# Kernel optimization log

Measured on AMD Instinct MI355X. Metric: run time of the kernel, lower is better.

The kernel has to match this reference:

```python
import jax, jax.numpy as jnp
import numpy as np
import math

H = 8
E = 512
D_K = E // H
NEG = -1000000000.0
# last (and only surviving) row of dist_bar: one threshold per head
DIST_BAR = np.array([0.2, 0.3, 0.4, 0.5, 0.6, 0.7, 0.8, 0.9], dtype=np.float32)


def setup_inputs() -> dict:
    key = jax.random.key(0)
    ks = jax.random.split(key, 12)
    B, N = 8, 1024
    s = 1.0 / math.sqrt(E)
    inp = {
        "query": jax.random.normal(ks[0], (B, N, E), jnp.float32),
        "key": jax.random.normal(ks[1], (B, N, E), jnp.float32),
        "value": jax.random.normal(ks[2], (B, N, E), jnp.float32),
        "dist": jax.random.uniform(ks[3], (B, 1, N, N), jnp.float32),
        "mask": jnp.ones((B, N, N), jnp.int32),
        "Wq": jax.random.normal(ks[4], (E, E), jnp.float32) * s,
        "bq": jnp.zeros((E,), jnp.float32),
        "Wk": jax.random.normal(ks[5], (E, E), jnp.float32) * s,
        "bk": jnp.zeros((E,), jnp.float32),
        "Wv": jax.random.normal(ks[6], (E, E), jnp.float32) * s,
        "bv": jnp.zeros((E,), jnp.float32),
        "Wo": jax.random.normal(ks[7], (E, E), jnp.float32) * s,
        "bo": jnp.zeros((E,), jnp.float32),
    }
    return inp


def reference(query, key, value, dist, mask, Wq, bq, Wk, bk, Wv, bv, Wo, bo):
    B, N, _ = query.shape
    # project and split heads: [B, H, N, D_K]
    def heads(x, W, b):
        return (x @ W.T + b).reshape(B, N, H, D_K).transpose(0, 2, 1, 3)
    q = heads(query, Wq, bq)
    k = heads(key, Wk, bk)
    v = heads(value, Wv, bv)
    scores = jnp.einsum("bhqd,bhkd->bhqk", q, k) / math.sqrt(D_K)
    # padding mask: [B,N,N] -> [B,1,N,N]
    scores = jnp.where(mask[:, None, :, :] == 0, NEG, scores)
    # per-head distance mask: dist [B,1,N,N] < thr[h] -> [B,H,N,N]
    thr = jnp.asarray(DIST_BAR)[None, :, None, None]
    dmask = dist < thr
    # first row/col (global atom) always attend
    dmask = dmask.at[:, :, 0, :].set(True).at[:, :, :, 0].set(True)
    scores = jnp.where(dmask, scores, NEG)
    p = jax.nn.softmax(scores, axis=-1)
    out = jnp.einsum("bhqk,bhkd->bhqd", p, v)  # [B,H,N,D_K]
    out = out.transpose(0, 2, 1, 3).reshape(B, N, H * D_K)
    return out @ Wo.T + bo
```

## Files before the change

### kernel.cpp

```cpp
#include <hip/hip_runtime.h>
#include <stdint.h>


typedef __attribute__((ext_vector_type(8))) short short8;
typedef __attribute__((ext_vector_type(4))) float floatx4;

#define MFMA16(a, b, c) __builtin_amdgcn_mfma_f32_16x16x32_bf16((a), (b), (c), 0, 0, 0)

static __device__ __forceinline__ unsigned short f2bf(float f) {
  union { float f; unsigned u; } v; v.f = f;
  unsigned r = v.u + 0x7fffu + ((v.u >> 16) & 1u);
  return (unsigned short)(r >> 16);
}

static __device__ __forceinline__ void gload_lds16(const void* g, void* l) {
  __builtin_amdgcn_global_load_lds((const __attribute__((address_space(1))) unsigned int*)g,
                                   (__attribute__((address_space(3))) unsigned int*)l,
                                   16, 0, 0);
}
static __device__ __forceinline__ int xsw(int row) { return (row & 3) ^ ((row >> 2) & 3); }

__global__ void codes_kernel(const float* __restrict__ dist, const int* __restrict__ mask,
                             unsigned char* __restrict__ codesP,
                             const float* __restrict__ Wq, const float* __restrict__ Wk,
                             const float* __restrict__ Wv, const float* __restrict__ Wo,
                             unsigned short* __restrict__ o0, unsigned short* __restrict__ o1,
                             unsigned short* __restrict__ o2, unsigned short* __restrict__ o3) {
  if (blockIdx.x >= 8192) {
    int i = (blockIdx.x - 8192) * blockDim.x + threadIdx.x;
    int w = i >> 16, loc = i & 65535;
    const float* s = (w == 0) ? Wq : (w == 1) ? Wk : (w == 2) ? Wv : Wo;
    unsigned short* d = (w == 0) ? o0 : (w == 1) ? o1 : (w == 2) ? o2 : o3;
    float4 v = ((const float4*)s)[loc];
    ushort4 o;
    o.x = f2bf(v.x); o.y = f2bf(v.y); o.z = f2bf(v.z); o.w = f2bf(v.w);
    ((ushort4*)d)[loc] = o;
    return;
  }
  int t = blockIdx.x * blockDim.x + threadIdx.x;
  int flat = t << 2;
  int b = flat >> 20;
  int rem = flat & ((1 << 20) - 1);
  int row = rem >> 10;
  int col0 = rem & 1023;
  float4 d4 = ((const float4*)dist)[t];
  int4 m4 = ((const int4*)mask)[t];
  float dv[4] = {d4.x, d4.y, d4.z, d4.w};
  int mv[4] = {m4.x, m4.y, m4.z, m4.w};
  int rg = row >> 5;
  int st = (row >> 4) & 1;
  int c = row & 15;
  size_t rowbase = (size_t)(b * 32 + rg) * 32768;
  int kt = col0 >> 7;
  int colk = col0 & 127;
  int ci = colk >> 4;
  int hi = (colk >> 2) & 3;
  int lane = hi * 16 + c;
  unsigned pack = 0;
#pragma unroll
  for (int u = 0; u < 4; u++) {
    int col = col0 + u;
    float d = dv[u];
    int hmin = (d >= 0.2f) + (d >= 0.3f) + (d >= 0.4f) + (d >= 0.5f) +
               (d >= 0.6f) + (d >= 0.7f) + (d >= 0.8f) + (d >= 0.9f);
    unsigned cc = (unsigned)hmin;
    if (row == 0 || col == 0) cc = 0;
    if (mv[u] == 0) cc = 9;
    pack |= cc << (u * 8);
  }
  *(unsigned*)&codesP[rowbase + (size_t)kt * 4096 + lane * 64 + st * 32 + ci * 4] = pack;
}

__global__ __launch_bounds__(256) void qkv_gemm(
    const float* __restrict__ Aq, const float* __restrict__ Ak, const float* __restrict__ Av,
    const unsigned short* __restrict__ Wqp, const unsigned short* __restrict__ Wkp,
    const unsigned short* __restrict__ Wvp,
    const float* __restrict__ bq, const float* __restrict__ bk, const float* __restrict__ bv,
    unsigned short* __restrict__ Qh, unsigned short* __restrict__ Kh,
    unsigned short* __restrict__ Vt) {
  const int z = blockIdx.z;
  const float* A = (z == 0) ? Aq : (z == 1) ? Ak : Av;
  const unsigned short* W = (z == 0) ? Wqp : (z == 1) ? Wkp : Wvp;
  const float* bias = (z == 0) ? bq : (z == 1) ? bk : bv;
  unsigned short* O = (z == 0) ? Qh : (z == 1) ? Kh : Vt;

  __shared__ __align__(16) short As[64 * 40];
  __shared__ __align__(16) short Bs[128 * 32];
  const int tid = threadIdx.x;
  const int lane = tid & 63;
  const int wave = tid >> 6;
  const int c = lane & 15;
  const int q = lane >> 4;
  const int m0 = blockIdx.x * 64;
  const int n0 = blockIdx.y * 128;
  const int wr = (wave >> 1) * 32;
  const int wc = (wave & 1) * 64;

  floatx4 acc[2][4];
#pragma unroll
  for (int i = 0; i < 2; i++)
#pragma unroll
    for (int j = 0; j < 4; j++) acc[i][j] = (floatx4)(0.0f);

  const int arow = tid >> 2, ach = tid & 3;
  const float* Ab = A + (size_t)(m0 + arow) * 512 + ach * 8;

  for (int k0 = 0; k0 < 512; k0 += 32) {
    __syncthreads();
#pragma unroll
    for (int it = 0; it < 2; it++) {
      int slot = wave * 128 + it * 64 + lane;
      int brow = slot >> 2, bch = slot & 3;
      int g = bch ^ xsw(brow);
      gload_lds16(W + (size_t)(n0 + brow) * 512 + k0 + g * 8,
                  &Bs[(size_t)(wave * 128 + it * 64) * 8]);
    }
    float4 a0 = *(const float4*)(Ab + k0);
    float4 a1 = *(const float4*)(Ab + k0 + 4);
    short8 av;
    av[0] = (short)f2bf(a0.x); av[1] = (short)f2bf(a0.y);
    av[2] = (short)f2bf(a0.z); av[3] = (short)f2bf(a0.w);
    av[4] = (short)f2bf(a1.x); av[5] = (short)f2bf(a1.y);
    av[6] = (short)f2bf(a1.z); av[7] = (short)f2bf(a1.w);
    *(short8*)(&As[arow * 40 + ach * 8]) = av;
    __syncthreads();

    short8 af[2], bfv[4];
#pragma unroll
    for (int i = 0; i < 2; i++)
      af[i] = *(const short8*)(&As[(wr + i * 16 + c) * 40 + q * 8]);
#pragma unroll
    for (int j = 0; j < 4; j++) {
      int row = wc + j * 16 + c;
      bfv[j] = *(const short8*)(&Bs[row * 32 + (q ^ xsw(row)) * 8]);
    }
#pragma unroll
    for (int i = 0; i < 2; i++)
#pragma unroll
      for (int j = 0; j < 4; j++)
        acc[i][j] = MFMA16(af[i], bfv[j], acc[i][j]);
  }

#pragma unroll
  for (int i = 0; i < 2; i++) {
    int gm0 = m0 + wr + i * 16 + q * 4;
#pragma unroll
    for (int j = 0; j < 4; j++) {
      int gn = n0 + wc + j * 16 + c;
      float bb = bias[gn];
      int h = gn >> 6, d = gn & 63;
      if (z == 2) {
        int b = gm0 >> 10, n = gm0 & 1023;
        ushort4 pk;
#pragma unroll
        for (int r = 0; r < 4; r++) pk[r] = f2bf(acc[i][j][r] + bb);
        *(ushort4*)(&Vt[(((size_t)(b * 8 + h) * 64 + d) << 10) + n]) = pk;
      } else {
#pragma unroll
        for (int r = 0; r < 4; r++) {
          int m = gm0 + r;
          int b = m >> 10, n = m & 1023;
          O[((((size_t)(b * 8 + h)) << 10) + n) * 64 + d] = f2bf(acc[i][j][r] + bb);
        }
      }
    }
  }
}

__global__ __launch_bounds__(256) void out_gemm(const unsigned short* __restrict__ A,
                                                const unsigned short* __restrict__ W,
                                                const float* __restrict__ bias,
                                                float* __restrict__ Out) {
  __shared__ __align__(16) short As[64 * 32];
  __shared__ __align__(16) short Bs[128 * 32];
  const int tid = threadIdx.x;
  const int lane = tid & 63;
  const int wave = tid >> 6;
  const int c = lane & 15;
  const int q = lane >> 4;
  const int m0 = blockIdx.x * 64;
  const int n0 = blockIdx.y * 128;
  const int wr = (wave >> 1) * 32;
  const int wc = (wave & 1) * 64;

  floatx4 acc[2][4];
#pragma unroll
  for (int i = 0; i < 2; i++)
#pragma unroll
    for (int j = 0; j < 4; j++) acc[i][j] = (floatx4)(0.0f);

  for (int k0 = 0; k0 < 512; k0 += 32) {
    __syncthreads();
    {
      int slot = wave * 64 + lane;
      int arow = slot >> 2, ach = slot & 3;
      int g = ach ^ xsw(arow);
      gload_lds16(A + (size_t)(m0 + arow) * 512 + k0 + g * 8, &As[(size_t)(wave * 64) * 8]);
    }
#pragma unroll
    for (int it = 0; it < 2; it++) {
      int slot = wave * 128 + it * 64 + lane;
      int brow = slot >> 2, bch = slot & 3;
      int g = bch ^ xsw(brow);
      gload_lds16(W + (size_t)(n0 + brow) * 512 + k0 + g * 8,
                  &Bs[(size_t)(wave * 128 + it * 64) * 8]);
    }
    __syncthreads();

    short8 af[2], bfv[4];
#pragma unroll
    for (int i = 0; i < 2; i++) {
      int row = wr + i * 16 + c;
      af[i] = *(const short8*)(&As[row * 32 + (q ^ xsw(row)) * 8]);
    }
#pragma unroll
    for (int j = 0; j < 4; j++) {
      int row = wc + j * 16 + c;
      bfv[j] = *(const short8*)(&Bs[row * 32 + (q ^ xsw(row)) * 8]);
    }
#pragma unroll
    for (int i = 0; i < 2; i++)
#pragma unroll
      for (int j = 0; j < 4; j++)
        acc[i][j] = MFMA16(af[i], bfv[j], acc[i][j]);
  }

#pragma unroll
  for (int i = 0; i < 2; i++) {
    int gm0 = m0 + wr + i * 16 + q * 4;
#pragma unroll
    for (int j = 0; j < 4; j++) {
      int gn = n0 + wc + j * 16 + c;
      float bb = bias[gn];
#pragma unroll
      for (int r = 0; r < 4; r++)
        Out[(size_t)(gm0 + r) * 512 + gn] = acc[i][j][r] + bb;
    }
  }
}

__global__ __launch_bounds__(256, 3) void attn_kernel(const unsigned short* __restrict__ Qh,
                                                      const unsigned short* __restrict__ Kh,
                                                      const unsigned short* __restrict__ Vt,
                                                      const unsigned char* __restrict__ codesP,
                                                      unsigned short* __restrict__ AO) {
  __shared__ __align__(16) unsigned short P[4][32 * 132];
  const int tid = threadIdx.x;
  const int lane = tid & 63;
  const int wave = tid >> 6;
  const int wsub = wave & 1;
  const int whalf = wave >> 1;
  const int c = lane & 15;
  const int q = lane >> 4;
  const int bid = blockIdx.x;
  const int swz = ((bid & 7) << 7) | (bid >> 3);
  const int bh = swz >> 4;
  const int gx = swz & 15;
  const int b = bh >> 3;
  const int h = bh & 7;
  const size_t base = (size_t)bh << 16;
  const int rbase = gx * 64 + wsub * 32;
  const int rg = rbase >> 5;
  unsigned short* Pw = &P[wave][0];

  short8 aq[2][2];
#pragma unroll
  for (int st = 0; st < 2; st++)
#pragma unroll
    for (int kk = 0; kk < 2; kk++)
      aq[st][kk] = *(const short8*)(Qh + base + (size_t)(rbase + st * 16 + c) * 64 + kk * 32 + q * 8);

  const unsigned char* cbt = codesP + (size_t)(b * 32 + rg) * 32768 + lane * 64;
  const unsigned short* Kb = Kh + base;
  const unsigned short* Vb = Vt + base;

  float rsum[2] = {0.0f, 0.0f};
  floatx4 o[2][4];
#pragma unroll
  for (int st = 0; st < 2; st++)
#pragma unroll
    for (int ci = 0; ci < 4; ci++) o[st][ci] = (floatx4)(0.0f);

  short8 bk00, bk01, bk10, bk11;
  {
    const unsigned short* Kt0 = Kb + (size_t)(whalf * 4) * 8192;
    bk00 = *(const short8*)(Kt0 + (size_t)(0 * 16 + c) * 64 + 0 * 32 + q * 8);
    bk01 = *(const short8*)(Kt0 + (size_t)(0 * 16 + c) * 64 + 1 * 32 + q * 8);
    bk10 = *(const short8*)(Kt0 + (size_t)(1 * 16 + c) * 64 + 0 * 32 + q * 8);
    bk11 = *(const short8*)(Kt0 + (size_t)(1 * 16 + c) * 64 + 1 * 32 + q * 8);
  }

#pragma unroll
  for (int ph = 0; ph < 16; ph++) {
    const int kt = whalf * 4 + (ph >> 2);
    const int j = ph & 3;
    const unsigned char* cp = cbt + (size_t)kt * 4096;

    short8 vv0 = *(const short8*)(Vb + (size_t)(0 * 16 + c) * 1024 + kt * 128 + j * 32 + q * 8);
    short8 vv1 = *(const short8*)(Vb + (size_t)(1 * 16 + c) * 1024 + kt * 128 + j * 32 + q * 8);
    short8 vv2 = *(const short8*)(Vb + (size_t)(2 * 16 + c) * 1024 + kt * 128 + j * 32 + q * 8);
    short8 vv3 = *(const short8*)(Vb + (size_t)(3 * 16 + c) * 1024 + kt * 128 + j * 32 + q * 8);
    uint2 cw0 = *(const uint2*)(cp + j * 8);
    uint2 cw1 = *(const uint2*)(cp + 32 + j * 8);

    floatx4 s2[2][2];
    s2[0][0] = (floatx4)(0.0f); s2[0][1] = (floatx4)(0.0f);
    s2[1][0] = (floatx4)(0.0f); s2[1][1] = (floatx4)(0.0f);
    s2[0][0] = MFMA16(bk00, aq[0][0], s2[0][0]);
    s2[1][0] = MFMA16(bk00, aq[1][0], s2[1][0]);
    s2[0][0] = MFMA16(bk01, aq[0][1], s2[0][0]);
    s2[1][0] = MFMA16(bk01, aq[1][1], s2[1][0]);
    s2[0][1] = MFMA16(bk10, aq[0][0], s2[0][1]);
    s2[1][1] = MFMA16(bk10, aq[1][0], s2[1][1]);
    s2[0][1] = MFMA16(bk11, aq[0][1], s2[0][1]);
    s2[1][1] = MFMA16(bk11, aq[1][1], s2[1][1]);

    if (ph < 15) {
      const int phn = ph + 1;
      const int ktn = whalf * 4 + (phn >> 2);
      const int jn = phn & 3;
      const unsigned short* Ktn = Kb + (size_t)ktn * 8192;
      bk00 = *(const short8*)(Ktn + (size_t)((2 * jn + 0) * 16 + c) * 64 + 0 * 32 + q * 8);
      bk01 = *(const short8*)(Ktn + (size_t)((2 * jn + 0) * 16 + c) * 64 + 1 * 32 + q * 8);
      bk10 = *(const short8*)(Ktn + (size_t)((2 * jn + 1) * 16 + c) * 64 + 0 * 32 + q * 8);
      bk11 = *(const short8*)(Ktn + (size_t)((2 * jn + 1) * 16 + c) * 64 + 1 * 32 + q * 8);
    }

#pragma unroll
    for (int st = 0; st < 2; st++) {
#pragma unroll
      for (int u = 0; u < 2; u++) {
        unsigned w = st ? (u ? cw1.y : cw1.x) : (u ? cw0.y : cw0.x);
        float ev[4];
#pragma unroll
        for (int r = 0; r < 4; r++) {
          int code = (w >> (r * 8)) & 0xff;
          float ee = (h >= code) ? exp2f(s2[st][u][r] * 0.1803368801111362f) : 0.0f;
          rsum[st] += ee;
          ev[r] = ee;
        }
        unsigned p0, p1;
        asm("v_cvt_pk_bf16_f32 %0, %1, %2" : "=v"(p0) : "v"(ev[0]), "v"(ev[1]));
        asm("v_cvt_pk_bf16_f32 %0, %1, %2" : "=v"(p1) : "v"(ev[2]), "v"(ev[3]));
        uint2 pk; pk.x = p0; pk.y = p1;
        *(uint2*)(&Pw[(st * 16 + c) * 132 + (2 * j + u) * 16 + q * 4]) = pk;
      }
    }

    __builtin_amdgcn_sched_barrier(0);

    short8 ap0 = *(const short8*)(&Pw[(size_t)c * 132 + j * 32 + q * 8]);
    short8 ap1 = *(const short8*)(&Pw[(size_t)(16 + c) * 132 + j * 32 + q * 8]);
    o[0][0] = MFMA16(ap0, vv0, o[0][0]);
    o[1][0] = MFMA16(ap1, vv0, o[1][0]);
    o[0][1] = MFMA16(ap0, vv1, o[0][1]);
    o[1][1] = MFMA16(ap1, vv1, o[1][1]);
    o[0][2] = MFMA16(ap0, vv2, o[0][2]);
    o[1][2] = MFMA16(ap1, vv2, o[1][2]);
    o[0][3] = MFMA16(ap0, vv3, o[0][3]);
    o[1][3] = MFMA16(ap1, vv3, o[1][3]);
  }

  float* Pf = (float*)&P[0][0];
  __syncthreads();
  if (whalf == 1) {
#pragma unroll
    for (int st = 0; st < 2; st++)
#pragma unroll
      for (int ci = 0; ci < 4; ci++)
        *(floatx4*)&Pf[(((wsub * 9 + st * 4 + ci) * 64) + lane) * 4] = o[st][ci];
    float2 rr; rr.x = rsum[0]; rr.y = rsum[1];
    *(float2*)&Pf[(((wsub * 9 + 8) * 64) + lane) * 4] = rr;
  }
  __syncthreads();
  if (whalf == 1) return;

#pragma unroll
  for (int st = 0; st < 2; st++)
#pragma unroll
    for (int ci = 0; ci < 4; ci++) {
      floatx4 p = *(const floatx4*)&Pf[(((wsub * 9 + st * 4 + ci) * 64) + lane) * 4];
      o[st][ci] += p;
    }
  {
    float2 pr = *(const float2*)&Pf[(((wsub * 9 + 8) * 64) + lane) * 4];
    rsum[0] += pr.x; rsum[1] += pr.y;
  }

  float inv2[2];
#pragma unroll
  for (int st = 0; st < 2; st++) {
    float v = rsum[st];
    v += __shfl_xor(v, 16);
    v += __shfl_xor(v, 32);
    inv2[st] = 1.0f / v;
  }
  const int sb = (lane & 48) + ((lane & 48) >> 2);
  float iv[2][4];
#pragma unroll
  for (int st = 0; st < 2; st++)
#pragma unroll
    for (int r = 0; r < 4; r++) iv[st][r] = __shfl(inv2[st], sb + r);

#pragma unroll
  for (int st = 0; st < 2; st++)
#pragma unroll
    for (int r = 0; r < 4; r++) {
      int n = rbase + st * 16 + q * 4 + r;
      size_t ob = ((size_t)((b << 10) + n)) * 512 + h * 64;
#pragma unroll
      for (int ci = 0; ci < 4; ci++)
        AO[ob + ci * 16 + c] = f2bf(o[st][ci][r] * iv[st][r]);
    }
}

extern "C" void kernel_launch(void* const* d_in, const int* in_sizes, int n_in,
                              void* d_out, int out_size, void* d_ws, size_t ws_size,
                              hipStream_t stream) {
  const float* query = (const float*)d_in[0];
  const float* key_  = (const float*)d_in[1];
  const float* value = (const float*)d_in[2];
  const float* dist  = (const float*)d_in[3];
  const int*   mask  = (const int*)d_in[4];
  const float* Wq = (const float*)d_in[5];
  const float* bq = (const float*)d_in[6];
  const float* Wk = (const float*)d_in[7];
  const float* bk = (const float*)d_in[8];
  const float* Wv = (const float*)d_in[9];
  const float* bv = (const float*)d_in[10];
  const float* Wo = (const float*)d_in[11];
  const float* bo = (const float*)d_in[12];

  char* ws = (char*)d_ws;
  size_t off = 0;
  auto alloc = [&](size_t bytes) -> char* {
    char* p = ws + off;
    off += (bytes + 255) & ~(size_t)255;
    return p;
  };
  const size_t NQKV = 8192ull * 512;
  unsigned short* wq16 = (unsigned short*)alloc(512ull * 512 * 2);
  unsigned short* wk16 = (unsigned short*)alloc(512ull * 512 * 2);
  unsigned short* wv16 = (unsigned short*)alloc(512ull * 512 * 2);
  unsigned short* wo16 = (unsigned short*)alloc(512ull * 512 * 2);
  unsigned short* Qh = (unsigned short*)alloc(NQKV * 2);
  unsigned short* Kh = (unsigned short*)alloc(NQKV * 2);
  unsigned short* Vt = (unsigned short*)alloc(NQKV * 2);
  unsigned short* AO = (unsigned short*)alloc(NQKV * 2);
  unsigned char*  codesP = (unsigned char*)alloc(8ull * 1024 * 1024);

  codes_kernel<<<9216, 256, 0, stream>>>(dist, mask, codesP, Wq, Wk, Wv, Wo,
                                         wq16, wk16, wv16, wo16);
  qkv_gemm<<<dim3(128, 4, 3), 256, 0, stream>>>(query, key_, value, wq16, wk16, wv16,
                                                bq, bk, bv, Qh, Kh, Vt);
  attn_kernel<<<1024, 256, 0, stream>>>(Qh, Kh, Vt, codesP, AO);
  out_gemm<<<dim3(128, 4), 256, 0, stream>>>(AO, wo16, bo, (float*)d_out);
}
```

Baseline: 277.4 us.

## Pre-convert QKV inputs to bf16 and coalesce codes writes through LDS

The prep kernel now also converts the query, key and value activations to bf16 in a separate pass. This lets qkv_gemm load its A tiles straight into LDS with global_load_lds and a swizzled layout, instead of converting fp32 in registers each k-step, so A is converted once rather than once per N-block. The codes computation is restructured so each block builds a 4 KB tile in shared memory and writes it out contiguously instead of scattering 4-byte stores. The cost is an extra bf16 copy of the inputs written to and read back from memory, plus extra workspace.

After: 275.7 us, median of 2. No clear change (-0.6%).

```diff
diff --git a/kernel.cpp b/kernel.cpp
--- a/kernel.cpp
+++ b/kernel.cpp
@@ -20,14 +20,36 @@
 }
 static __device__ __forceinline__ int xsw(int row) { return (row & 3) ^ ((row >> 2) & 3); }
 
-__global__ void codes_kernel(const float* __restrict__ dist, const int* __restrict__ mask,
-                             unsigned char* __restrict__ codesP,
-                             const float* __restrict__ Wq, const float* __restrict__ Wk,
-                             const float* __restrict__ Wv, const float* __restrict__ Wo,
-                             unsigned short* __restrict__ o0, unsigned short* __restrict__ o1,
-                             unsigned short* __restrict__ o2, unsigned short* __restrict__ o3) {
-  if (blockIdx.x >= 8192) {
-    int i = (blockIdx.x - 8192) * blockDim.x + threadIdx.x;
+__global__ void prep_kernel(const float* __restrict__ dist, const int* __restrict__ mask,
+                            unsigned char* __restrict__ codesP,
+                            const float* __restrict__ Wq, const float* __restrict__ Wk,
+                            const float* __restrict__ Wv, const float* __restrict__ Wo,
+                            unsigned short* __restrict__ o0, unsigned short* __restrict__ o1,
+                            unsigned short* __restrict__ o2, unsigned short* __restrict__ o3,
+                            const float* __restrict__ Qf, const float* __restrict__ Kf,
+                            const float* __restrict__ Vf,
+                            unsigned short* __restrict__ Qb, unsigned short* __restrict__ Kb,
+                            unsigned short* __restrict__ Vb) {
+  const int tid = threadIdx.x;
+  const unsigned bx = blockIdx.x;
+  if (bx >= 3072) {
+    int j = bx - 3072;
+    int arr = j >> 11;
+    const float* s = (arr == 0) ? Qf : (arr == 1) ? Kf : Vf;
+    unsigned short* d = (arr == 0) ? Qb : (arr == 1) ? Kb : Vb;
+    int idx = (j & 2047) * 256 + tid;
+    float4 v0 = ((const float4*)s)[idx * 2];
+    float4 v1 = ((const float4*)s)[idx * 2 + 1];
+    short8 o;
+    o[0] = (short)f2bf(v0.x); o[1] = (short)f2bf(v0.y);
+    o[2] = (short)f2bf(v0.z); o[3] = (short)f2bf(v0.w);
+    o[4] = (short)f2bf(v1.x); o[5] = (short)f2bf(v1.y);
+    o[6] = (short)f2bf(v1.z); o[7] = (short)f2bf(v1.w);
+    *(short8*)(d + (size_t)idx * 8) = o;
+    return;
+  }
+  if (bx >= 2048) {
+    int i = (bx - 2048) * 256 + tid;
     int w = i >> 16, loc = i & 65535;
     const float* s = (w == 0) ? Wq : (w == 1) ? Wk : (w == 2) ? Wv : Wo;
     unsigned short* d = (w == 0) ? o0 : (w == 1) ? o1 : (w == 2) ? o2 : o3;
@@ -37,54 +59,61 @@
     ((ushort4*)d)[loc] = o;
     return;
   }
-  int t = blockIdx.x * blockDim.x + threadIdx.x;
-  int flat = t << 2;
-  int b = flat >> 20;
-  int rem = flat & ((1 << 20) - 1);
-  int row = rem >> 10;
-  int col0 = rem & 1023;
-  float4 d4 = ((const float4*)dist)[t];
-  int4 m4 = ((const int4*)mask)[t];
-  float dv[4] = {d4.x, d4.y, d4.z, d4.w};
-  int mv[4] = {m4.x, m4.y, m4.z, m4.w};
-  int rg = row >> 5;
-  int st = (row >> 4) & 1;
-  int c = row & 15;
-  size_t rowbase = (size_t)(b * 32 + rg) * 32768;
-  int kt = col0 >> 7;
-  int colk = col0 & 127;
-  int ci = colk >> 4;
-  int hi = (colk >> 2) & 3;
-  int lane = hi * 16 + c;
-  unsigned pack = 0;
-#pragma unroll
-  for (int u = 0; u < 4; u++) {
-    int col = col0 + u;
-    float d = dv[u];
-    int hmin = (d >= 0.2f) + (d >= 0.3f) + (d >= 0.4f) + (d >= 0.5f) +
-               (d >= 0.6f) + (d >= 0.7f) + (d >= 0.8f) + (d >= 0.9f);
-    unsigned cc = (unsigned)hmin;
-    if (row == 0 || col == 0) cc = 0;
-    if (mv[u] == 0) cc = 9;
-    pack |= cc << (u * 8);
-  }
-  *(unsigned*)&codesP[rowbase + (size_t)kt * 4096 + lane * 64 + st * 32 + ci * 4] = pack;
+  __shared__ __align__(16) unsigned char cbuf[4096];
+  const int bc = bx;
+  const int b = bc >> 8;
+  const int rg = (bc >> 3) & 31;
+  const int kt = bc & 7;
+  const int row_local = tid >> 3;
+  const int colseg = (tid & 7) * 16;
+  const int row = rg * 32 + row_local;
+  const int st = row_local >> 4;
+  const int c = row_local & 15;
+  const int ci = tid & 7;
+  const size_t ibase = ((size_t)b << 20) + (size_t)row * 1024 + kt * 128 + colseg;
+  float4 d4[4]; int4 m4[4];
+#pragma unroll
+  for (int g = 0; g < 4; g++) {
+    d4[g] = ((const float4*)(dist + ibase))[g];
+    m4[g] = ((const int4*)(mask + ibase))[g];
+  }
+#pragma unroll
+  for (int hi = 0; hi < 4; hi++) {
+    float dvv[4] = {d4[hi].x, d4[hi].y, d4[hi].z, d4[hi].w};
+    int mvv[4] = {m4[hi].x, m4[hi].y, m4[hi].z, m4[hi].w};
+    unsigned pack = 0;
+#pragma unroll
+    for (int r = 0; r < 4; r++) {
+      int col = kt * 128 + colseg + hi * 4 + r;
+      float d = dvv[r];
+      int hmin = (d >= 0.2f) + (d >= 0.3f) + (d >= 0.4f) + (d >= 0.5f) +
+                 (d >= 0.6f) + (d >= 0.7f) + (d >= 0.8f) + (d >= 0.9f);
+      unsigned cc = (unsigned)hmin;
+      if (row == 0 || col == 0) cc = 0;
+      if (mvv[r] == 0) cc = 9;
+      pack |= cc << (r * 8);
+    }
+    *(unsigned*)&cbuf[(hi * 16 + c) * 64 + st * 32 + ci * 4] = pack;
+  }
+  __syncthreads();
+  *(uint4*)&codesP[(size_t)bc * 4096 + tid * 16] = *(const uint4*)&cbuf[tid * 16];
 }
 
 __global__ __launch_bounds__(256) void qkv_gemm(
-    const float* __restrict__ Aq, const float* __restrict__ Ak, const float* __restrict__ Av,
+    const unsigned short* __restrict__ Aq, const unsigned short* __restrict__ Ak,
+    const unsigned short* __restrict__ Av,
     const unsigned short* __restrict__ Wqp, const unsigned short* __restrict__ Wkp,
     const unsigned short* __restrict__ Wvp,
     const float* __restrict__ bq, const float* __restrict__ bk, const float* __restrict__ bv,
     unsigned short* __restrict__ Qh, unsigned short* __restrict__ Kh,
     unsigned short* __restrict__ Vt) {
   const int z = blockIdx.z;
-  const float* A = (z == 0) ? Aq : (z == 1) ? Ak : Av;
+  const unsigned short* A = (z == 0) ? Aq : (z == 1) ? Ak : Av;
   const unsigned short* W = (z == 0) ? Wqp : (z == 1) ? Wkp : Wvp;
   const float* bias = (z == 0) ? bq : (z == 1) ? bk : bv;
   unsigned short* O = (z == 0) ? Qh : (z == 1) ? Kh : Vt;
 
-  __shared__ __align__(16) short As[64 * 40];
+  __shared__ __align__(16) short As[64 * 32];
   __shared__ __align__(16) short Bs[128 * 32];
   const int tid = threadIdx.x;
   const int lane = tid & 63;
@@ -102,11 +131,14 @@
 #pragma unroll
     for (int j = 0; j < 4; j++) acc[i][j] = (floatx4)(0.0f);
 
-  const int arow = tid >> 2, ach = tid & 3;
-  const float* Ab = A + (size_t)(m0 + arow) * 512 + ach * 8;
-
   for (int k0 = 0; k0 < 512; k0 += 32) {
     __syncthreads();
+    {
+      int slot = wave * 64 + lane;
+      int arow = slot >> 2, ach = slot & 3;
+      int g = ach ^ xsw(arow);
+      gload_lds16(A + (size_t)(m0 + arow) * 512 + k0 + g * 8, &As[(size_t)(wave * 64) * 8]);
+    }
 #pragma unroll
     for (int it = 0; it < 2; it++) {
       int slot = wave * 128 + it * 64 + lane;
@@ -115,20 +147,14 @@
       gload_lds16(W + (size_t)(n0 + brow) * 512 + k0 + g * 8,
                   &Bs[(size_t)(wave * 128 + it * 64) * 8]);
     }
-    float4 a0 = *(const float4*)(Ab + k0);
-    float4 a1 = *(const float4*)(Ab + k0 + 4);
-    short8 av;
-    av[0] = (short)f2bf(a0.x); av[1] = (short)f2bf(a0.y);
-    av[2] = (short)f2bf(a0.z); av[3] = (short)f2bf(a0.w);
-    av[4] = (short)f2bf(a1.x); av[5] = (short)f2bf(a1.y);
-    av[6] = (short)f2bf(a1.z); av[7] = (short)f2bf(a1.w);
-    *(short8*)(&As[arow * 40 + ach * 8]) = av;
     __syncthreads();
 
     short8 af[2], bfv[4];
 #pragma unroll
-    for (int i = 0; i < 2; i++)
-      af[i] = *(const short8*)(&As[(wr + i * 16 + c) * 40 + q * 8]);
+    for (int i = 0; i < 2; i++) {
+      int row = wr + i * 16 + c;
+      af[i] = *(const short8*)(&As[row * 32 + (q ^ xsw(row)) * 8]);
+    }
 #pragma unroll
     for (int j = 0; j < 4; j++) {
       int row = wc + j * 16 + c;
@@ -448,10 +474,14 @@
   unsigned short* Vt = (unsigned short*)alloc(NQKV * 2);
   unsigned short* AO = (unsigned short*)alloc(NQKV * 2);
   unsigned char*  codesP = (unsigned char*)alloc(8ull * 1024 * 1024);
-
-  codes_kernel<<<9216, 256, 0, stream>>>(dist, mask, codesP, Wq, Wk, Wv, Wo,
-                                         wq16, wk16, wv16, wo16);
-  qkv_gemm<<<dim3(128, 4, 3), 256, 0, stream>>>(query, key_, value, wq16, wk16, wv16,
+  unsigned short* Qi = (unsigned short*)alloc(NQKV * 2);
+  unsigned short* Ki = (unsigned short*)alloc(NQKV * 2);
+  unsigned short* Vi = (unsigned short*)alloc(NQKV * 2);
+
+  prep_kernel<<<9216, 256, 0, stream>>>(dist, mask, codesP, Wq, Wk, Wv, Wo,
+                                        wq16, wk16, wv16, wo16,
+                                        query, key_, value, Qi, Ki, Vi);
+  qkv_gemm<<<dim3(128, 4, 3), 256, 0, stream>>>(Qi, Ki, Vi, wq16, wk16, wv16,
                                                 bq, bk, bv, Qh, Kh, Vt);
   attn_kernel<<<1024, 256, 0, stream>>>(Qh, Kh, Vt, codesP, AO);
   out_gemm<<<dim3(128, 4), 256, 0, stream>>>(AO, wo16, bo, (float*)d_out);
```
